# Kernel tuning notes

Measured on AMD Instinct MI355X. Metric: run time of the kernel, lower is better.

Reference implementation:

```python
import jax, jax.numpy as jnp
import numpy as np

L, E, H, FF, N, S, ML = 6, 768, 12, 3072, 8, 1023, 2048


def setup_inputs() -> dict:
    key = jax.random.key(0)
    ks = jax.random.split(key, 16)
    rn = lambda k, shape, s=0.02: jax.random.normal(k, shape, jnp.float32) * s
    return {
        "x": jax.random.normal(ks[0], (N, S, E), jnp.float32),
        "mask": jnp.ones((N, 1, 1, S + 1), jnp.int32),
        "pos_emb": rn(ks[1], (ML, E), 1.0),
        "cls": rn(ks[2], (1, 1, E), 1.0),
        "Wq": rn(ks[3], (L, E, E)), "bq": jnp.zeros((L, E), jnp.float32),
        "Wk": rn(ks[4], (L, E, E)), "bk": jnp.zeros((L, E), jnp.float32),
        "Wv": rn(ks[5], (L, E, E)), "bv": jnp.zeros((L, E), jnp.float32),
        "Wo": rn(ks[6], (L, E, E)), "bo": jnp.zeros((L, E), jnp.float32),
        "ln1_g": jnp.ones((L, E), jnp.float32), "ln1_b": jnp.zeros((L, E), jnp.float32),
        "ln2_g": jnp.ones((L, E), jnp.float32), "ln2_b": jnp.zeros((L, E), jnp.float32),
        "Wf1": rn(ks[7], (L, E, FF)), "bf1": jnp.zeros((L, FF), jnp.float32),
        "Wf2": rn(ks[8], (L, FF, E)), "bf2": jnp.zeros((L, E), jnp.float32),
    }


def _ln(x, g, b, eps=1e-5):
    m = x.mean(-1, keepdims=True)
    v = ((x - m) ** 2).mean(-1, keepdims=True)
    return (x - m) / jnp.sqrt(v + eps) * g + b


def reference(x, mask, pos_emb, cls, Wq, bq, Wk, bk, Wv, bv, Wo, bo,
              ln1_g, ln1_b, ln2_g, ln2_b, Wf1, bf1, Wf2, bf2):
    n, s, e = x.shape
    h = H
    d = e // h
    # prepend CLS token -> [N, T, E], add learned positions
    x = jnp.concatenate([jnp.broadcast_to(cls, (n, 1, e)), x], axis=1)
    t = s + 1
    out = x + pos_emb[:t][None]
    scale = jnp.float32(1.0 / np.sqrt(d))
    for i in range(Wq.shape[0]):
        q = (out @ Wq[i] + bq[i]).reshape(n, t, h, d)
        k = (out @ Wk[i] + bk[i]).reshape(n, t, h, d)
        v = (out @ Wv[i] + bv[i]).reshape(n, t, h, d)
        energy = jnp.einsum('nqhd,nkhd->nhqk', q, k)  # [N,H,T,T]
        energy = jnp.where(mask == 0, jnp.float32(-1e20), energy)
        attn = jax.nn.softmax(energy * scale, axis=-1)
        att = jnp.einsum('nhqk,nkhd->nqhd', attn, v).reshape(n, t, e)
        att = att @ Wo[i] + bo[i]
        hid = _ln(att + out, ln1_g[i], ln1_b[i])  # residual uses query (=out)
        ff = jax.nn.gelu(hid @ Wf1[i] + bf1[i], approximate=False) @ Wf2[i] + bf2[i]
        out = _ln(ff + hid, ln2_g[i], ln2_b[i])
    return out
```

## Files before the change

kernel.cpp:

```cpp
#include <hip/hip_runtime.h>

#define L_ 6
#define E_ 768
#define H_ 12
#define FF_ 3072

typedef __attribute__((ext_vector_type(8))) short bh8;
typedef __attribute__((ext_vector_type(4))) float f32x4;

__device__ inline ushort f2bf(float f) {
  unsigned u = __builtin_bit_cast(unsigned, f);
  u += 0x7fffu + ((u >> 16) & 1u);
  return (ushort)(u >> 16);
}
__device__ inline float bf2f(ushort h) {
  return __builtin_bit_cast(float, (unsigned)h << 16);
}

__device__ __forceinline__ void gload16(const void* g, void* l) {
  __builtin_amdgcn_global_load_lds(
      (const __attribute__((address_space(1))) void*)g,
      (__attribute__((address_space(3))) void*)l, 16, 0, 0);
}

__global__ __launch_bounds__(256) void pack_bias(const float* __restrict__ bq,
                                                 const float* __restrict__ bk,
                                                 const float* __restrict__ bv,
                                                 float* __restrict__ bqkv) {
  int idx = blockIdx.x * 256 + threadIdx.x;
  int l = idx / 2304, j = idx % 2304;
  float v = (j < 768) ? bq[l * 768 + j]
          : (j < 1536) ? bk[l * 768 + j - 768]
                       : bv[l * 768 + j - 1536];
  bqkv[idx] = v;
}

__global__ __launch_bounds__(256) void transpose_w(const float* __restrict__ src,
                                                   ushort* __restrict__ dst,
                                                   int K, int Nn,
                                                   long sstride, long dstride) {
  src += (long)blockIdx.z * sstride;
  dst += (long)blockIdx.z * dstride;
  __shared__ float t[32][33];
  int tx = threadIdx.x & 31, ty = threadIdx.x >> 5;
  int kb = blockIdx.x * 32, nb = blockIdx.y * 32;
#pragma unroll
  for (int i = 0; i < 4; i++) {
    int kr = ty + i * 8;
    t[kr][tx] = src[(long)(kb + kr) * Nn + nb + tx];
  }
  __syncthreads();
#pragma unroll
  for (int i = 0; i < 4; i++) {
    int nr = ty + i * 8;
    dst[(long)(nb + nr) * K + kb + tx] = f2bf(t[tx][nr]);
  }
}

__global__ __launch_bounds__(256) void embed_k(const float* __restrict__ x,
                                               const float* __restrict__ pos,
                                               const float* __restrict__ cls,
                                               float* __restrict__ res,
                                               ushort* __restrict__ xb) {
  int idx = blockIdx.x * 256 + threadIdx.x;
  int c4 = idx % 192;
  int row = idx / 192;
  int t = row & 1023, n = row >> 10;
  f32x4 pv = ((const f32x4*)pos)[t * 192 + c4];
  f32x4 xv;
  if (t == 0) xv = ((const f32x4*)cls)[c4];
  else        xv = ((const f32x4*)x)[(size_t)(n * 1023 + t - 1) * 192 + c4];
  f32x4 s = xv + pv;
  ((f32x4*)res)[idx] = s;
  ushort4 h;
  h.x = f2bf(s[0]); h.y = f2bf(s[1]); h.z = f2bf(s[2]); h.w = f2bf(s[3]);
  ((ushort4*)xb)[idx] = h;
}

template <int MODE>
__global__ __launch_bounds__(256, 4) void gemm_bt(const ushort* __restrict__ A,
                                                  const ushort* __restrict__ Bt,
                                                  int M, int N, int K,
                                                  const float* __restrict__ bias,
                                                  ushort* __restrict__ sp0,
                                                  ushort* __restrict__ sp1,
                                                  ushort* __restrict__ sp2,
                                                  ushort* __restrict__ sp3,
                                                  ushort* __restrict__ out16,
                                                  ushort* __restrict__ vtb,
                                                  int ksl) {
  __shared__ ushort As[128 * 64];
  __shared__ ushort Bs[128 * 64];
  int tid = threadIdx.x;
  int wid = tid >> 6, lane = tid & 63;
  int wm = wid >> 1, wn = wid & 1;
  int l15 = lane & 15, lhi = lane >> 4;
  int ln8 = lane >> 3, lc8 = (lane & 7) * 8;
  int row0 = blockIdx.x * 128, col0 = blockIdx.y * 128;
  int kb = (MODE == 3) ? blockIdx.z * ksl : 0;
  int nt = ((MODE == 3) ? ksl : K) >> 6;

  f32x4 acc[4][4];
#pragma unroll
  for (int i = 0; i < 4; i++)
#pragma unroll
    for (int j = 0; j < 4; j++) acc[i][j] = (f32x4){0.f, 0.f, 0.f, 0.f};

  const ushort* Ap = A + (size_t)(row0 + wid * 32 + ln8) * K + kb + lc8;
  const ushort* Bp = Bt + (size_t)(col0 + wid * 32 + ln8) * K + kb + lc8;

  for (int kt = 0; kt < nt; ++kt) {
    int k0 = kt << 6;
#pragma unroll
    for (int p = 0; p < 4; p++) {
      int r = wid * 32 + p * 8;
      gload16(Ap + (size_t)p * 8 * K + k0, As + r * 64);
      gload16(Bp + (size_t)p * 8 * K + k0, Bs + r * 64);
    }
    __syncthreads();
#pragma unroll
    for (int ks = 0; ks < 2; ks++) {
      bh8 af[4], bfr[4];
#pragma unroll
      for (int i = 0; i < 4; i++)
        af[i] = *(const bh8*)(As + (wm * 64 + i * 16 + l15) * 64 + ks * 32 + lhi * 8);
#pragma unroll
      for (int j = 0; j < 4; j++)
        bfr[j] = *(const bh8*)(Bs + (wn * 64 + j * 16 + l15) * 64 + ks * 32 + lhi * 8);
#pragma unroll
      for (int i = 0; i < 4; i++)
#pragma unroll
        for (int j = 0; j < 4; j++)
          acc[i][j] = __builtin_amdgcn_mfma_f32_16x16x32_bf16(af[i], bfr[j], acc[i][j], 0, 0, 0);
    }
    __syncthreads();
  }

  ushort* outp = nullptr;
  if (MODE == 3)
    outp = (blockIdx.z == 0) ? sp0 : (blockIdx.z == 1) ? sp1 : (blockIdx.z == 2) ? sp2 : sp3;
#pragma unroll
  for (int j = 0; j < 4; j++) {
    int col = col0 + wn * 64 + j * 16 + l15;
    float bv = (MODE == 3) ? 0.f : bias[col];
#pragma unroll
    for (int i = 0; i < 4; i++) {
      int rbase = row0 + wm * 64 + i * 16 + lhi * 4;
      if (MODE == 0 && col >= 1536) {
        int hd = col - 1536;
        int nn = rbase >> 10, t0 = rbase & 1023;
        ushort4 h4;
        h4.x = f2bf(acc[i][j][0] + bv);
        h4.y = f2bf(acc[i][j][1] + bv);
        h4.z = f2bf(acc[i][j][2] + bv);
        h4.w = f2bf(acc[i][j][3] + bv);
        *(ushort4*)(vtb + ((size_t)nn * 768 + hd) * 1024 + t0) = h4;
      } else {
#pragma unroll
        for (int r = 0; r < 4; r++) {
          int row = rbase + r;
          size_t o = (size_t)row * N + col;
          float v = acc[i][j][r] + bv;
          if (MODE == 0) {
            out16[o] = f2bf(v);
          } else if (MODE == 3) {
            outp[o] = f2bf(v);
          } else {
            v = 0.5f * v * (1.f + erff(v * 0.70710678118f));
            out16[o] = f2bf(v);
          }
        }
      }
    }
  }
}

__global__ __launch_bounds__(512, 1) void gemm256s(const ushort* __restrict__ A,
                                                   const ushort* __restrict__ Bt,
                                                   int M, int N, int K,
                                                   ushort* __restrict__ sp0,
                                                   ushort* __restrict__ sp1,
                                                   int ksl) {
  extern __shared__ ushort smem[];
  int tid = threadIdx.x;
  int wid = tid >> 6, lane = tid & 63;
  int wr = wid >> 2, wc = wid & 3;
  int l15 = lane & 15, lhi = lane >> 4;
  int x7 = l15 & 7;
  int row0 = blockIdx.x * 256, col0 = blockIdx.y * 256;
  int kb = blockIdx.z * ksl;
  int nt = ksl >> 6;

  int srow = tid >> 3;
  int swk = ((tid & 7) ^ (srow & 7)) << 3;
  const ushort* Ag = A + (size_t)(row0 + srow) * K + kb + swk;
  const ushort* Bg = Bt + (size_t)(col0 + srow) * K + kb + swk;

  auto stA = [&](int slot, int kt, int half) {
#pragma unroll
    for (int it = 0; it < 2; ++it) {
      int gr0 = half * 128 + it * 64;
      gload16(Ag + (size_t)gr0 * K + (size_t)kt * 64,
              smem + (slot << 14) + (gr0 + wid * 8) * 64);
    }
  };
  auto stB = [&](int slot, int kt, int half) {
#pragma unroll
    for (int it = 0; it < 2; ++it) {
      int gr0 = half * 128 + it * 64;
      gload16(Bg + (size_t)gr0 * K + (size_t)kt * 64,
              smem + 32768 + (slot << 14) + (gr0 + wid * 8) * 64);
    }
  };

  f32x4 acc[8][4];
#pragma unroll
  for (int i = 0; i < 8; i++)
#pragma unroll
    for (int j = 0; j < 4; j++) acc[i][j] = (f32x4){0.f, 0.f, 0.f, 0.f};

  stB(0, 0, 0); stB(0, 0, 1);
  stA(0, 0, 0); stA(0, 0, 1);
  stB(1, 1, 0); stB(1, 1, 1);

  bh8 bfr[4][2];

  for (int t = 0; t < nt; ++t) {
    int s = t & 1;
    const ushort* Ab = smem + (s << 14);
    const ushort* Bb = smem + 32768 + (s << 14);

    if (t + 1 < nt) {
      stA(s ^ 1, t + 1, 0);
      asm volatile("s_waitcnt vmcnt(6)" ::: "memory");
    } else {
      asm volatile("s_waitcnt vmcnt(0)" ::: "memory");
    }
    __builtin_amdgcn_s_barrier();

#pragma unroll
    for (int j = 0; j < 4; ++j)
#pragma unroll
      for (int kk = 0; kk < 2; ++kk)
        bfr[j][kk] = *(const bh8*)(Bb + (wc * 64 + j * 16 + l15) * 64 +
                                   (((kk * 4 + lhi) ^ x7) << 3));
    {
      bh8 af[2][2];
#pragma unroll
      for (int il = 0; il < 2; ++il)
#pragma unroll
        for (int kk = 0; kk < 2; ++kk)
          af[il][kk] = *(const bh8*)(Ab + (wr * 128 + il * 16 + l15) * 64 +
                                     (((kk * 4 + lhi) ^ x7) << 3));
      __builtin_amdgcn_s_setprio(1);
#pragma unroll
      for (int il = 0; il < 2; ++il)
#pragma unroll
        for (int j = 0; j < 4; ++j)
#pragma unroll
          for (int kk = 0; kk < 2; ++kk)
            acc[il][j] = __builtin_amdgcn_mfma_f32_16x16x32_bf16(
                af[il][kk], bfr[j][kk], acc[il][j], 0, 0, 0);
      __builtin_amdgcn_s_setprio(0);
    }
    asm volatile("s_waitcnt lgkmcnt(0)" ::: "memory");
    __builtin_amdgcn_s_barrier();

    if (t + 1 < nt) stA(s ^ 1, t + 1, 1);
    if (t + 2 < nt) stB(s, t + 2, 0);
#pragma unroll
    for (int q = 1; q < 4; ++q) {
      if (q == 2 && t + 2 < nt) stB(s, t + 2, 1);
      bh8 af[2][2];
#pragma unroll
      for (int il = 0; il < 2; ++il)
#pragma unroll
        for (int kk = 0; kk < 2; ++kk)
          af[il][kk] = *(const bh8*)(Ab + (wr * 128 + (q * 2 + il) * 16 + l15) * 64 +
                                     (((kk * 4 + lhi) ^ x7) << 3));
      __builtin_amdgcn_s_setprio(1);
#pragma unroll
      for (int il = 0; il < 2; ++il)
#pragma unroll
        for (int j = 0; j < 4; ++j)
#pragma unroll
          for (int kk = 0; kk < 2; ++kk)
            acc[q * 2 + il][j] = __builtin_amdgcn_mfma_f32_16x16x32_bf16(
                af[il][kk], bfr[j][kk], acc[q * 2 + il][j], 0, 0, 0);
      __builtin_amdgcn_s_setprio(0);
    }
  }

  ushort* outp = (blockIdx.z == 0) ? sp0 : sp1;
#pragma unroll
  for (int j = 0; j < 4; j++) {
    int col = col0 + wc * 64 + j * 16 + l15;
#pragma unroll
    for (int i = 0; i < 8; i++) {
      int rbase = row0 + wr * 128 + i * 16 + lhi * 4;
#pragma unroll
      for (int r = 0; r < 4; r++) {
        size_t o = (size_t)(rbase + r) * N + col;
        outp[o] = f2bf(acc[i][j][r]);
      }
    }
  }
}

__global__ __launch_bounds__(512) void attn_k(const ushort* __restrict__ qkv,
                                              const ushort* __restrict__ vtb,
                                              const int* __restrict__ mask,
                                              ushort* __restrict__ attb) {
  int qt = blockIdx.x, h = blockIdx.y, n = blockIdx.z;
  int tid = threadIdx.x, wid = tid >> 6, lane = tid & 63;
  int l15 = lane & 15, lhi = lane >> 4;
  __shared__ ushort Ks[2][64 * 64];
  __shared__ ushort Vs[2][64 * 64];
  __shared__ ushort Pt[8][16 * 64];
  ushort* Pw = Pt[wid];

  int ln8 = lane >> 3;
  int swc = (((lane & 7) ^ ln8) << 3);

  const ushort* Kg = qkv + 768 + h * 64;
  const ushort* Vg = vtb + (size_t)(n * 768 + h * 64) * 1024;

  auto stage = [&](int b, int kv0) {
    int r = wid * 8;
    gload16(Kg + (size_t)(n * 1024 + kv0 + r + ln8) * 2304 + swc, &Ks[b][r * 64]);
    gload16(Vg + (size_t)(r + ln8) * 1024 + kv0 + swc, &Vs[b][r * 64]);
  };

  stage(0, 0);

  int q0 = qt * 128 + wid * 16;
  size_t rowQ = (size_t)(n * 1024 + q0 + l15) * 2304 + h * 64;
  bh8 qf0 = *(const bh8*)(qkv + rowQ + lhi * 8);
  bh8 qf1 = *(const bh8*)(qkv + rowQ + 32 + lhi * 8);

  unsigned long long mbits = 0ull;
#pragma unroll
  for (int i = 0; i < 64; ++i)
    mbits |= (unsigned long long)(mask[n * 1024 + i * 16 + l15] != 0) << i;

  bh8 ones;
#pragma unroll
  for (int i = 0; i < 8; ++i) ones[i] = (short)0x3F80;

  f32x4 o[4], lacc = (f32x4){0.f, 0.f, 0.f, 0.f};
#pragma unroll
  for (int i = 0; i < 4; i++) o[i] = (f32x4){0.f, 0.f, 0.f, 0.f};

  int x15 = (l15 & 7) << 3;
  int buf = 0;
  for (int t = 0; t < 16; ++t) {
    if (t < 15) {
      stage(buf ^ 1, (t + 1) * 64);
      asm volatile("s_waitcnt vmcnt(2)" ::: "memory");
    } else {
      asm volatile("s_waitcnt vmcnt(0)" ::: "memory");
    }
    __builtin_amdgcn_s_barrier();
    const ushort* Kb = Ks[buf];
    const ushort* Vb = Vs[buf];

    f32x4 s[4];
    __builtin_amdgcn_s_setprio(1);
#pragma unroll
    for (int t4 = 0; t4 < 4; ++t4) {
      int rs = (t4 * 16 + l15) * 64;
      s[t4] = (f32x4){0.f, 0.f, 0.f, 0.f};
      s[t4] = __builtin_amdgcn_mfma_f32_16x16x32_bf16(qf0, *(const bh8*)(Kb + rs + ((lhi << 3) ^ x15)), s[t4], 0, 0, 0);
      s[t4] = __builtin_amdgcn_mfma_f32_16x16x32_bf16(qf1, *(const bh8*)(Kb + rs + (((4 + lhi) << 3) ^ x15)), s[t4], 0, 0, 0);
    }
    __builtin_amdgcn_s_setprio(0);

#pragma unroll
    for (int t4 = 0; t4 < 4; ++t4) {
      bool mk = (mbits >> (t * 4 + t4)) & 1ull;
#pragma unroll
      for (int r = 0; r < 4; r++) {
        float xv = mk ? s[t4][r] * 0.125f : -1e20f;
        float p = __expf(fminf(xv, 80.f));
        int prow = lhi * 4 + r;
        int slot = t4 * 2 + (l15 >> 3);
        Pw[prow * 64 + (((slot ^ (prow & 7)) << 3) | (l15 & 7))] = f2bf(p);
      }
    }

    bh8 pf0 = *(const bh8*)(Pw + l15 * 64 + ((lhi << 3) ^ x15));
    bh8 pf1 = *(const bh8*)(Pw + l15 * 64 + (((4 + lhi) << 3) ^ x15));
    __builtin_amdgcn_s_setprio(1);
#pragma unroll
    for (int nb = 0; nb < 4; nb++) {
      int rs = (nb * 16 + l15) * 64;
      o[nb] = __builtin_amdgcn_mfma_f32_16x16x32_bf16(pf0, *(const bh8*)(Vb + rs + ((lhi << 3) ^ x15)), o[nb], 0, 0, 0);
      o[nb] = __builtin_amdgcn_mfma_f32_16x16x32_bf16(pf1, *(const bh8*)(Vb + rs + (((4 + lhi) << 3) ^ x15)), o[nb], 0, 0, 0);
    }
    lacc = __builtin_amdgcn_mfma_f32_16x16x32_bf16(pf0, ones, lacc, 0, 0, 0);
    lacc = __builtin_amdgcn_mfma_f32_16x16x32_bf16(pf1, ones, lacc, 0, 0, 0);
    __builtin_amdgcn_s_setprio(0);

    if (t < 15) {
      asm volatile("s_waitcnt lgkmcnt(0)" ::: "memory");
      __builtin_amdgcn_s_barrier();
    }
    buf ^= 1;
  }

#pragma unroll
  for (int nb = 0; nb < 4; nb++)
#pragma unroll
    for (int r = 0; r < 4; r++) {
      float val = o[nb][r] / lacc[r];
      int row = q0 + lhi * 4 + r;
      int col = h * 64 + nb * 16 + l15;
      attb[(size_t)(n * 1024 + row) * 768 + col] = f2bf(val);
    }
}

template <int S>
__global__ __launch_bounds__(256) void ln_red_k(const ushort* __restrict__ p0,
                                                const ushort* __restrict__ p1,
                                                const ushort* __restrict__ p2,
                                                const ushort* __restrict__ p3,
                                                const float* __restrict__ resid,
                                                const float* __restrict__ bias,
                                                const float* __restrict__ g,
                                                const float* __restrict__ b,
                                                float* __restrict__ y32,
                                                ushort* __restrict__ y16) {
  int row = blockIdx.x, tid = threadIdx.x;
  size_t base = (size_t)row * 768;
  float v[3];
#pragma unroll
  for (int i = 0; i < 3; i++) {
    int c = tid + i * 256;
    float s = resid[base + c] + bias[c];
    s += bf2f(p0[base + c]);
    if (S > 1) s += bf2f(p1[base + c]);
    if (S > 2) s += bf2f(p2[base + c]);
    if (S > 3) s += bf2f(p3[base + c]);
    v[i] = s;
  }
  float s = v[0] + v[1] + v[2];
  float sq = v[0] * v[0] + v[1] * v[1] + v[2] * v[2];
#pragma unroll
  for (int off = 32; off > 0; off >>= 1) {
    s += __shfl_down(s, off);
    sq += __shfl_down(sq, off);
  }
  __shared__ float sws[4], swq[4];
  int wid = tid >> 6, lane = tid & 63;
  if (lane == 0) { sws[wid] = s; swq[wid] = sq; }
  __syncthreads();
  float ts = sws[0] + sws[1] + sws[2] + sws[3];
  float tq = swq[0] + swq[1] + swq[2] + swq[3];
  float mean = ts * (1.f / 768.f);
  float var = tq * (1.f / 768.f) - mean * mean;
  float rstd = rsqrtf(var + 1e-5f);
#pragma unroll
  for (int i = 0; i < 3; i++) {
    int c = tid + i * 256;
    float y = (v[i] - mean) * rstd * g[c] + b[c];
    y32[base + c] = y;
    y16[base + c] = f2bf(y);
  }
}

extern "C" void kernel_launch(void* const* d_in, const int* in_sizes, int n_in,
                              void* d_out, int out_size, void* d_ws, size_t ws_size,
                              hipStream_t stream) {
  const float* x    = (const float*)d_in[0];
  const int*   mask = (const int*)d_in[1];
  const float* pos  = (const float*)d_in[2];
  const float* cls  = (const float*)d_in[3];
  const float* Wq   = (const float*)d_in[4];
  const float* bq   = (const float*)d_in[5];
  const float* Wk   = (const float*)d_in[6];
  const float* bk   = (const float*)d_in[7];
  const float* Wv   = (const float*)d_in[8];
  const float* bv   = (const float*)d_in[9];
  const float* Wo   = (const float*)d_in[10];
  const float* bo   = (const float*)d_in[11];
  const float* ln1g = (const float*)d_in[12];
  const float* ln1b = (const float*)d_in[13];
  const float* ln2g = (const float*)d_in[14];
  const float* ln2b = (const float*)d_in[15];
  const float* Wf1  = (const float*)d_in[16];
  const float* bf1  = (const float*)d_in[17];
  const float* Wf2  = (const float*)d_in[18];
  const float* bf2w = (const float*)d_in[19];

  hipFuncSetAttribute(reinterpret_cast<const void*>(gemm256s),
                      hipFuncAttributeMaxDynamicSharedMemorySize, 131072);

  char* ws = (char*)d_ws;
  size_t off = 0;
  auto alloc = [&](size_t bytes) {
    char* p = ws + off;
    off += (bytes + 255) & ~(size_t)255;
    return p;
  };
  const size_t M = 8192;
  ushort* qkvt = (ushort*)alloc((size_t)L_ * 2304 * 768 * 2);
  ushort* wot  = (ushort*)alloc((size_t)L_ * 768 * 768 * 2);
  ushort* wf1t = (ushort*)alloc((size_t)L_ * 3072 * 768 * 2);
  ushort* wf2t = (ushort*)alloc((size_t)L_ * 768 * 3072 * 2);
  float*  bqkv = (float*)alloc((size_t)L_ * 2304 * 4);
  float*  res  = (float*)alloc(M * 768 * 4);
  float*  pre  = (float*)alloc(M * 768 * 4);
  ushort* xb   = (ushort*)alloc(M * 768 * 2);
  ushort* qkvb = (ushort*)alloc(M * 2304 * 2);
  ushort* vtb  = (ushort*)alloc(M * 768 * 2);
  ushort* attb = (ushort*)alloc(M * 768 * 2);
  ushort* ffb  = (ushort*)alloc(M * 3072 * 2);
  (void)ws_size; (void)in_sizes; (void)n_in; (void)out_size;

  ushort* slA = (ushort*)pre;
  ushort* slB = slA + M * 768;
  ushort* slC = (ushort*)qkvb;
  ushort* slD = slC + M * 768;

  dim3 tb(256);
  pack_bias<<<54, tb, 0, stream>>>(bq, bk, bv, bqkv);
  transpose_w<<<dim3(24, 24, 6), tb, 0, stream>>>(Wq, qkvt,              768, 768, 768L * 768, 2304L * 768);
  transpose_w<<<dim3(24, 24, 6), tb, 0, stream>>>(Wk, qkvt + 768 * 768,  768, 768, 768L * 768, 2304L * 768);
  transpose_w<<<dim3(24, 24, 6), tb, 0, stream>>>(Wv, qkvt + 2 * 768 * 768, 768, 768, 768L * 768, 2304L * 768);
  transpose_w<<<dim3(24, 24, 6), tb, 0, stream>>>(Wo, wot, 768, 768, 768L * 768, 768L * 768);
  transpose_w<<<dim3(24, 96, 6), tb, 0, stream>>>(Wf1, wf1t, 768, 3072, 768L * 3072, 3072L * 768);
  transpose_w<<<dim3(96, 24, 6), tb, 0, stream>>>(Wf2, wf2t, 3072, 768, 3072L * 768, 768L * 3072);
  embed_k<<<6144, tb, 0, stream>>>(x, pos, cls, res, xb);

  for (int l = 0; l < L_; l++) {
    gemm_bt<0><<<dim3(64, 18), tb, 0, stream>>>(xb, qkvt + (size_t)l * 2304 * 768,
                                                8192, 2304, 768, bqkv + l * 2304,
                                                nullptr, nullptr, nullptr, nullptr,
                                                qkvb, vtb, 0);
    attn_k<<<dim3(8, 12, 8), dim3(512), 0, stream>>>(qkvb, vtb, mask, attb);
    gemm_bt<3><<<dim3(64, 6, 4), tb, 0, stream>>>(attb, wot + (size_t)l * 768 * 768,
                                                  8192, 768, 768, nullptr,
                                                  slA, slB, slC, slD,
                                                  nullptr, nullptr, 192);
    ln_red_k<4><<<8192, tb, 0, stream>>>(slA, slB, slC, slD, res, bo + l * 768,
                                         ln1g + l * 768, ln1b + l * 768, res, xb);
    gemm_bt<2><<<dim3(64, 24), tb, 0, stream>>>(xb, wf1t + (size_t)l * 3072 * 768,
                                                8192, 3072, 768, bf1 + l * 3072,
                                                nullptr, nullptr, nullptr, nullptr,
                                                ffb, nullptr, 0);
    float* y32 = (l == L_ - 1) ? (float*)d_out : res;
    gemm256s<<<dim3(32, 3, 2), 512, 131072, stream>>>(ffb, wf2t + (size_t)l * 768 * 3072,
                                                      8192, 768, 3072,
                                                      slA, slB, 1536);
    ln_red_k<2><<<8192, tb, 0, stream>>>(slA, slB, nullptr, nullptr, res, bf2w + l * 768,
                                         ln2g + l * 768, ln2b + l * 768, y32, xb);
  }
}
```

Measured before the change: 1.827 ms.

## Keep residual stream in bf16, halve out-proj split-K, vectorize layernorm

Drops the fp32 residual buffer and reads the residual from the bf16 activation copy (xb) in both layernorm kernels. The layernorm kernel is rewritten to 192 threads with 4-wide vector loads and stores, and writes only the needed output (bf16 for inner layers, fp32 for the final one). The output-projection GEMM's split-K goes from 4 to 2, so fewer partial buffers are written and reduced. The aim is to cut memory traffic in the reduction/layernorm kernels, at the cost of bf16 rounding accumulating in the residual path and larger per-block work in the out-proj GEMM.

```diff
diff --git a/kernel.cpp b/kernel.cpp
--- a/kernel.cpp
+++ b/kernel.cpp
@@ -60,7 +60,6 @@
 __global__ __launch_bounds__(256) void embed_k(const float* __restrict__ x,
                                                const float* __restrict__ pos,
                                                const float* __restrict__ cls,
-                                               float* __restrict__ res,
                                                ushort* __restrict__ xb) {
   int idx = blockIdx.x * 256 + threadIdx.x;
   int c4 = idx % 192;
@@ -71,7 +70,6 @@
   if (t == 0) xv = ((const f32x4*)cls)[c4];
   else        xv = ((const f32x4*)x)[(size_t)(n * 1023 + t - 1) * 192 + c4];
   f32x4 s = xv + pv;
-  ((f32x4*)res)[idx] = s;
   ushort4 h;
   h.x = f2bf(s[0]); h.y = f2bf(s[1]); h.z = f2bf(s[2]); h.w = f2bf(s[3]);
   ((ushort4*)xb)[idx] = h;
@@ -84,8 +82,6 @@
                                                   const float* __restrict__ bias,
                                                   ushort* __restrict__ sp0,
                                                   ushort* __restrict__ sp1,
-                                                  ushort* __restrict__ sp2,
-                                                  ushort* __restrict__ sp3,
                                                   ushort* __restrict__ out16,
                                                   ushort* __restrict__ vtb,
                                                   int ksl) {
@@ -137,8 +133,7 @@
   }
 
   ushort* outp = nullptr;
-  if (MODE == 3)
-    outp = (blockIdx.z == 0) ? sp0 : (blockIdx.z == 1) ? sp1 : (blockIdx.z == 2) ? sp2 : sp3;
+  if (MODE == 3) outp = (blockIdx.z == 0) ? sp0 : sp1;
 #pragma unroll
   for (int j = 0; j < 4; j++) {
     int col = col0 + wn * 64 + j * 16 + l15;
@@ -419,52 +414,55 @@
     }
 }
 
-template <int S>
-__global__ __launch_bounds__(256) void ln_red_k(const ushort* __restrict__ p0,
+template <bool FINAL>
+__global__ __launch_bounds__(192) void ln_red_k(const ushort* __restrict__ p0,
                                                 const ushort* __restrict__ p1,
-                                                const ushort* __restrict__ p2,
-                                                const ushort* __restrict__ p3,
-                                                const float* __restrict__ resid,
+                                                const ushort* __restrict__ resid,
                                                 const float* __restrict__ bias,
                                                 const float* __restrict__ g,
                                                 const float* __restrict__ b,
                                                 float* __restrict__ y32,
                                                 ushort* __restrict__ y16) {
   int row = blockIdx.x, tid = threadIdx.x;
-  size_t base = (size_t)row * 768;
-  float v[3];
-#pragma unroll
-  for (int i = 0; i < 3; i++) {
-    int c = tid + i * 256;
-    float s = resid[base + c] + bias[c];
-    s += bf2f(p0[base + c]);
-    if (S > 1) s += bf2f(p1[base + c]);
-    if (S > 2) s += bf2f(p2[base + c]);
-    if (S > 3) s += bf2f(p3[base + c]);
-    v[i] = s;
-  }
-  float s = v[0] + v[1] + v[2];
-  float sq = v[0] * v[0] + v[1] * v[1] + v[2] * v[2];
+  int c = tid * 4;
+  size_t base = (size_t)row * 768 + c;
+  ushort4 r4 = *(const ushort4*)(resid + base);
+  ushort4 a4 = *(const ushort4*)(p0 + base);
+  ushort4 q4 = *(const ushort4*)(p1 + base);
+  float4 bi = *(const float4*)(bias + c);
+  float v[4];
+  v[0] = bf2f(r4.x) + bf2f(a4.x) + bf2f(q4.x) + bi.x;
+  v[1] = bf2f(r4.y) + bf2f(a4.y) + bf2f(q4.y) + bi.y;
+  v[2] = bf2f(r4.z) + bf2f(a4.z) + bf2f(q4.z) + bi.z;
+  v[3] = bf2f(r4.w) + bf2f(a4.w) + bf2f(q4.w) + bi.w;
+  float s = v[0] + v[1] + v[2] + v[3];
+  float sq = v[0] * v[0] + v[1] * v[1] + v[2] * v[2] + v[3] * v[3];
 #pragma unroll
   for (int off = 32; off > 0; off >>= 1) {
     s += __shfl_down(s, off);
     sq += __shfl_down(sq, off);
   }
-  __shared__ float sws[4], swq[4];
-  int wid = tid >> 6, lane = tid & 63;
-  if (lane == 0) { sws[wid] = s; swq[wid] = sq; }
+  __shared__ float sws[3], swq[3];
+  int wd = tid >> 6, lane = tid & 63;
+  if (lane == 0) { sws[wd] = s; swq[wd] = sq; }
   __syncthreads();
-  float ts = sws[0] + sws[1] + sws[2] + sws[3];
-  float tq = swq[0] + swq[1] + swq[2] + swq[3];
+  float ts = sws[0] + sws[1] + sws[2];
+  float tq = swq[0] + swq[1] + swq[2];
   float mean = ts * (1.f / 768.f);
   float var = tq * (1.f / 768.f) - mean * mean;
   float rstd = rsqrtf(var + 1e-5f);
-#pragma unroll
-  for (int i = 0; i < 3; i++) {
-    int c = tid + i * 256;
-    float y = (v[i] - mean) * rstd * g[c] + b[c];
-    y32[base + c] = y;
-    y16[base + c] = f2bf(y);
+  float4 g4 = *(const float4*)(g + c);
+  float4 b4 = *(const float4*)(b + c);
+  float y0 = (v[0] - mean) * rstd * g4.x + b4.x;
+  float y1 = (v[1] - mean) * rstd * g4.y + b4.y;
+  float y2 = (v[2] - mean) * rstd * g4.z + b4.z;
+  float y3 = (v[3] - mean) * rstd * g4.w + b4.w;
+  if (FINAL) {
+    *(float4*)(y32 + base) = make_float4(y0, y1, y2, y3);
+  } else {
+    ushort4 h;
+    h.x = f2bf(y0); h.y = f2bf(y1); h.z = f2bf(y2); h.w = f2bf(y3);
+    *(ushort4*)(y16 + base) = h;
   }
 }
 
@@ -508,19 +506,14 @@
   ushort* wf1t = (ushort*)alloc((size_t)L_ * 3072 * 768 * 2);
   ushort* wf2t = (ushort*)alloc((size_t)L_ * 768 * 3072 * 2);
   float*  bqkv = (float*)alloc((size_t)L_ * 2304 * 4);
-  float*  res  = (float*)alloc(M * 768 * 4);
-  float*  pre  = (float*)alloc(M * 768 * 4);
   ushort* xb   = (ushort*)alloc(M * 768 * 2);
   ushort* qkvb = (ushort*)alloc(M * 2304 * 2);
   ushort* vtb  = (ushort*)alloc(M * 768 * 2);
   ushort* attb = (ushort*)alloc(M * 768 * 2);
   ushort* ffb  = (ushort*)alloc(M * 3072 * 2);
+  ushort* slA  = (ushort*)alloc(M * 768 * 2 * 2);
+  ushort* slB  = slA + M * 768;
   (void)ws_size; (void)in_sizes; (void)n_in; (void)out_size;
-
-  ushort* slA = (ushort*)pre;
-  ushort* slB = slA + M * 768;
-  ushort* slC = (ushort*)qkvb;
-  ushort* slD = slC + M * 768;
 
   dim3 tb(256);
   pack_bias<<<54, tb, 0, stream>>>(bq, bk, bv, bqkv);
@@ -530,29 +523,33 @@
   transpose_w<<<dim3(24, 24, 6), tb, 0, stream>>>(Wo, wot, 768, 768, 768L * 768, 768L * 768);
   transpose_w<<<dim3(24, 96, 6), tb, 0, stream>>>(Wf1, wf1t, 768, 3072, 768L * 3072, 3072L * 768);
   transpose_w<<<dim3(96, 24, 6), tb, 0, stream>>>(Wf2, wf2t, 3072, 768, 3072L * 768, 768L * 3072);
-  embed_k<<<6144, tb, 0, stream>>>(x, pos, cls, res, xb);
+  embed_k<<<6144, tb, 0, stream>>>(x, pos, cls, xb);
 
   for (int l = 0; l < L_; l++) {
     gemm_bt<0><<<dim3(64, 18), tb, 0, stream>>>(xb, qkvt + (size_t)l * 2304 * 768,
                                                 8192, 2304, 768, bqkv + l * 2304,
-                                                nullptr, nullptr, nullptr, nullptr,
-                                                qkvb, vtb, 0);
+                                                nullptr, nullptr, qkvb, vtb, 0);
     attn_k<<<dim3(8, 12, 8), dim3(512), 0, stream>>>(qkvb, vtb, mask, attb);
-    gemm_bt<3><<<dim3(64, 6, 4), tb, 0, stream>>>(attb, wot + (size_t)l * 768 * 768,
+    gemm_bt<3><<<dim3(64, 6, 2), tb, 0, stream>>>(attb, wot + (size_t)l * 768 * 768,
                                                   8192, 768, 768, nullptr,
-                                                  slA, slB, slC, slD,
-                                                  nullptr, nullptr, 192);
-    ln_red_k<4><<<8192, tb, 0, stream>>>(slA, slB, slC, slD, res, bo + l * 768,
-                                         ln1g + l * 768, ln1b + l * 768, res, xb);
+                                                  slA, slB, nullptr, nullptr, 384);
+    ln_red_k<false><<<8192, dim3(192), 0, stream>>>(slA, slB, xb, bo + l * 768,
+                                                    ln1g + l * 768, ln1b + l * 768,
+                                                    nullptr, xb);
     gemm_bt<2><<<dim3(64, 24), tb, 0, stream>>>(xb, wf1t + (size_t)l * 3072 * 768,
                                                 8192, 3072, 768, bf1 + l * 3072,
-                                                nullptr, nullptr, nullptr, nullptr,
-                                                ffb, nullptr, 0);
-    float* y32 = (l == L_ - 1) ? (float*)d_out : res;
+                                                nullptr, nullptr, ffb, nullptr, 0);
     gemm256s<<<dim3(32, 3, 2), 512, 131072, stream>>>(ffb, wf2t + (size_t)l * 768 * 3072,
                                                       8192, 768, 3072,
                                                       slA, slB, 1536);
-    ln_red_k<2><<<8192, tb, 0, stream>>>(slA, slB, nullptr, nullptr, res, bf2w + l * 768,
-                                         ln2g + l * 768, ln2b + l * 768, y32, xb);
-  }
-}
+    if (l < L_ - 1) {
+      ln_red_k<false><<<8192, dim3(192), 0, stream>>>(slA, slB, xb, bf2w + l * 768,
+                                                      ln2g + l * 768, ln2b + l * 768,
+                                                      nullptr, xb);
+    } else {
+      ln_red_k<true><<<8192, dim3(192), 0, stream>>>(slA, slB, xb, bf2w + l * 768,
+                                                     ln2g + l * 768, ln2b + l * 768,
+                                                     (float*)d_out, nullptr);
+    }
+  }
+}
```

New measurement: 1.656 ms. 1.1x faster.
